# Optimization experiments

Hardware: AMD Instinct MI355X
Metric: run time of the kernel (lower is better)

Reference implementation:

```python
import jax, jax.numpy as jnp
import numpy as np

DIM = 2048       # model dim
HID = 1024       # expert hidden dim
E = 8            # num_experts
K = 2            # top_k
SHID = HID * 1   # shared expert hidden = hidden_dim * num_shared_experts
INIT = 0.02


def setup_inputs() -> dict:
    key = jax.random.key(0)
    ks = jax.random.split(key, 9)
    return {
        "x": jax.random.normal(ks[0], (2, 1024, DIM), jnp.float32),
        "expert_bias": jnp.zeros((E,), jnp.float32),
        "gate_w": jax.random.normal(ks[1], (E, DIM), jnp.float32) * INIT,
        "w1": jax.random.normal(ks[2], (E, HID, DIM), jnp.float32) * INIT,
        "w2": jax.random.normal(ks[3], (E, DIM, HID), jnp.float32) * INIT,
        "w3": jax.random.normal(ks[4], (E, HID, DIM), jnp.float32) * INIT,
        "sw1": jax.random.normal(ks[5], (SHID, DIM), jnp.float32) * INIT,
        "sw2": jax.random.normal(ks[6], (DIM, SHID), jnp.float32) * INIT,
        "sw3": jax.random.normal(ks[7], (SHID, DIM), jnp.float32) * INIT,
    }


def reference(x, expert_bias, gate_w, w1, w2, w3, sw1, sw2, sw3):
    B, S, D = x.shape
    xf = x.reshape(-1, D)                      # [N, D]
    N = xf.shape[0]

    # --- TokenChoiceTopKRouter (sigmoid score, bias-adjusted top-k selection) ---
    scores = jax.nn.sigmoid((xf @ gate_w.T).astype(jnp.float32))      # [N, E]
    _, sel = jax.lax.top_k(scores + expert_bias[None, :], K)          # [N, K] indices
    top_scores = jnp.take_along_axis(scores, sel, axis=1)             # [N, K] (route_norm=False, route_scale=1.0)

    # --- TokenReorderer: stable sort routed slots by expert id ---
    flat_exp = sel.reshape(-1)                                        # [N*K]
    order = jnp.argsort(flat_exp, stable=True)                        # expert-sorted slot order
    sorted_exp = flat_exp[order]                                      # [N*K]
    tok_idx = order // K                                              # source token per slot
    sc_sorted = top_scores.reshape(-1)[order]                         # [N*K]

    # score_before_experts=True: scale input by routing score before expert FFN
    rin = xf[tok_idx] * sc_sorted[:, None].astype(x.dtype)            # [N*K, D]

    # --- GroupedExperts: per-expert SwiGLU on the expert-sorted token block ---
    # (grouped GEMM expressed as a masked loop over the fixed expert set)
    out_sorted = jnp.zeros_like(rin)
    for e in range(E):
        m = (sorted_exp == e)[:, None].astype(rin.dtype)
        h = jax.nn.silu(rin @ w1[e].T) * (rin @ w3[e].T)              # [N*K, HID]
        out_sorted = out_sorted + m * (h @ w2[e].T)

    # combine: scatter-add expert outputs back to tokens
    routed = jnp.zeros((N, D), x.dtype).at[tok_idx].add(out_sorted)

    # shared expert (plain SwiGLU FeedForward)
    shared = (jax.nn.silu(xf @ sw1.T) * (xf @ sw3.T)) @ sw2.T

    return (routed + shared).reshape(B, S, D)
```

## Files before the change

### kernel.cpp

```cpp
#include <hip/hip_runtime.h>
#include <hip/hip_bf16.h>
#include <stdint.h>

#define DIMM 2048
#define HIDD 1024
#define NEXP 8
#define TOPK 2
#define NTOK 2048
#define CAP_E 1024
#define CAP_T (NEXP * CAP_E)

typedef __bf16 bf16_t;
typedef __bf16 bf16x4 __attribute__((ext_vector_type(4)));
typedef __bf16 bf16x8 __attribute__((ext_vector_type(8)));
typedef float f32x4 __attribute__((ext_vector_type(4)));

__device__ __forceinline__ void gl2lds16(const bf16_t* g, bf16_t* l) {
    __builtin_amdgcn_global_load_lds(
        (const __attribute__((address_space(1))) void*)g,
        (__attribute__((address_space(3))) void*)l, 16, 0, 0);
}

__global__ __launch_bounds__(256) void conv_f2b(const float* __restrict__ s,
                                                bf16_t* __restrict__ d, int n4) {
    int i = blockIdx.x * 256 + threadIdx.x;
    if (i >= n4) return;
    float4 v = ((const float4*)s)[i];
    bf16x4 o = {(bf16_t)v.x, (bf16_t)v.y, (bf16_t)v.z, (bf16_t)v.w};
    ((bf16x4*)d)[i] = o;
}

__global__ __launch_bounds__(256) void conv_w13(const float* __restrict__ w1,
                                                const float* __restrict__ w3,
                                                bf16_t* __restrict__ d, int n4) {
    int i = blockIdx.x * 256 + threadIdx.x;
    if (i >= n4) return;
    long flat = (long)i * 4;
    int e = (int)(flat >> 22);
    int rem = (int)(flat & ((1 << 22) - 1));
    int r = rem >> 11;
    int dd = rem & 2047;
    const float* src = (r < HIDD)
        ? (w1 + ((long)e << 21) + ((long)r << 11) + dd)
        : (w3 + ((long)e << 21) + ((long)(r - HIDD) << 11) + dd);
    float4 v = *(const float4*)src;
    bf16x4 o = {(bf16_t)v.x, (bf16_t)v.y, (bf16_t)v.z, (bf16_t)v.w};
    ((bf16x4*)d)[i] = o;
}

__global__ __launch_bounds__(256) void router_k(const float* __restrict__ x,
                                                const float* __restrict__ gw,
                                                const float* __restrict__ bias,
                                                int* __restrict__ sel,
                                                float* __restrict__ topsc) {
    int t = blockIdx.x;
    int tid = threadIdx.x;
    const float* xr = x + (long)t * DIMM;
    double acc[NEXP];
#pragma unroll
    for (int e = 0; e < NEXP; ++e) acc[e] = 0.0;
    for (int d = tid; d < DIMM; d += 256) {
        double xv = (double)xr[d];
#pragma unroll
        for (int e = 0; e < NEXP; ++e) acc[e] += xv * (double)gw[e * DIMM + d];
    }
#pragma unroll
    for (int off = 32; off >= 1; off >>= 1)
#pragma unroll
        for (int e = 0; e < NEXP; ++e) acc[e] += __shfl_down(acc[e], off, 64);
    __shared__ double red[4][NEXP];
    int lane = tid & 63, w = tid >> 6;
    if (lane == 0)
#pragma unroll
        for (int e = 0; e < NEXP; ++e) red[w][e] = acc[e];
    __syncthreads();
    if (tid == 0) {
        double sc[NEXP], v[NEXP];
#pragma unroll
        for (int e = 0; e < NEXP; ++e) {
            double s = red[0][e] + red[1][e] + red[2][e] + red[3][e];
            sc[e] = 1.0 / (1.0 + exp(-s));
            v[e] = sc[e] + (double)bias[e];
        }
        int b0 = 0;
        for (int e = 1; e < NEXP; ++e) if (v[e] > v[b0]) b0 = e;
        int b1 = -1;
        for (int e = 0; e < NEXP; ++e)
            if (e != b0 && (b1 < 0 || v[e] > v[b1])) b1 = e;
        sel[t * 2] = b0; sel[t * 2 + 1] = b1;
        topsc[t * 2] = (float)sc[b0]; topsc[t * 2 + 1] = (float)sc[b1];
    }
}

__global__ __launch_bounds__(256) void sort_k(const int* __restrict__ sel,
                                              const float* __restrict__ topsc,
                                              int* __restrict__ tok_s,
                                              float* __restrict__ sc_s,
                                              int* __restrict__ counts) {
    __shared__ int se[NTOK * TOPK];
    int tid = threadIdx.x;
    for (int i = tid; i < NTOK * TOPK; i += 256) se[i] = sel[i];
    __syncthreads();
    int wv = tid >> 6, lane = tid & 63;
    unsigned long long lower = (1ull << lane) - 1ull;
    for (int ei = 0; ei < 2; ++ei) {
        int e = wv * 2 + ei;
        int base = e * CAP_E;
        int off = 0;
        for (int c = 0; c < (NTOK * TOPK) / 64; ++c) {
            int slot = c * 64 + lane;
            bool m = (se[slot] == e);
            unsigned long long bal = __ballot(m);
            if (m) {
                int rank = off + __popcll(bal & lower);
                if (rank < CAP_E) {
                    tok_s[base + rank] = slot >> 1;
                    sc_s[base + rank] = topsc[slot];
                }
            }
            off += __popcll(bal);
        }
        int cnt = min(off, CAP_E);
        if (lane == 0) counts[e] = cnt;
        int padded = min((cnt + 127) & ~127, CAP_E);
        for (int r = cnt + lane; r < padded; r += 64) tok_s[base + r] = -1;
    }
}

__global__ __launch_bounds__(256) void build_rin(const float* __restrict__ x,
                                                 const int* __restrict__ tok_s,
                                                 const float* __restrict__ sc_s,
                                                 const int* __restrict__ counts,
                                                 bf16_t* __restrict__ rin) {
    int row = blockIdx.x;
    int e = row >> 10, r = row & (CAP_E - 1);
    int cnt = min(counts[e], CAP_E);
    int padded = min((cnt + 127) & ~127, CAP_E);
    if (r >= padded) return;
    int d0 = threadIdx.x * 8;
    bf16x8 o;
    if (r < cnt) {
        int tok = tok_s[row];
        float sc = sc_s[row];
        const float* src = x + (long)tok * DIMM + d0;
        float4 a = *(const float4*)src;
        float4 b = *(const float4*)(src + 4);
        o[0] = (bf16_t)(a.x * sc); o[1] = (bf16_t)(a.y * sc);
        o[2] = (bf16_t)(a.z * sc); o[3] = (bf16_t)(a.w * sc);
        o[4] = (bf16_t)(b.x * sc); o[5] = (bf16_t)(b.y * sc);
        o[6] = (bf16_t)(b.z * sc); o[7] = (bf16_t)(b.w * sc);
    } else {
#pragma unroll
        for (int i = 0; i < 8; ++i) o[i] = (bf16_t)0.0f;
    }
    *(bf16x8*)(rin + (long)row * DIMM + d0) = o;
}

template <int EPI>
__global__ __launch_bounds__(256, 2) void gemm_bt(
    const bf16_t* __restrict__ A0, const bf16_t* __restrict__ B0,
    void* __restrict__ C0, const int* __restrict__ counts, int Mfixed,
    int N, int K, long sA, long sB, long sC,
    const int* __restrict__ tok_s, float* __restrict__ outp) {
    int e = blockIdx.z;
    int M = Mfixed;
    if (counts) {
        int c = min(counts[e], Mfixed);
        M = min((c + 127) & ~127, Mfixed);
    }
    int m0 = blockIdx.y * 128;
    if (m0 >= M) return;
    int n0 = blockIdx.x * 128;
    const bf16_t* A = A0 + (long)e * sA;
    const bf16_t* B = B0 + (long)e * sB;

    __shared__ bf16_t lA[128 * 64];
    __shared__ bf16_t lB[128 * 64];

    int tid = threadIdx.x;
    int lane = tid & 63, wv = tid >> 6;
    int quad = lane >> 4, l16 = lane & 15;
    int wm = (wv & 1) * 64, wn = (wv >> 1) * 64;

    f32x4 acc[4][4];
#pragma unroll
    for (int i = 0; i < 4; ++i)
#pragma unroll
        for (int j = 0; j < 4; ++j) acc[i][j] = (f32x4){0.f, 0.f, 0.f, 0.f};

    int kTiles = K >> 6;
    for (int kt = 0; kt < kTiles; ++kt) {
        int kb = kt << 6;
#pragma unroll
        for (int i = 0; i < 4; ++i) {
            int q = i * 256 + tid;
            int row = q >> 3, cc = q & 7;
            int scc = cc ^ (row & 7);
            gl2lds16(A + (long)(m0 + row) * K + kb + scc * 8, &lA[q * 8]);
            gl2lds16(B + (long)(n0 + row) * K + kb + scc * 8, &lB[q * 8]);
        }
        __syncthreads();
#pragma unroll
        for (int ki = 0; ki < 2; ++ki) {
            bf16x8 af[4], bfr[4];
            int kc = ki * 4 + quad;
#pragma unroll
            for (int mi = 0; mi < 4; ++mi) {
                int row = wm + mi * 16 + l16;
                int chunk = row * 8 + (kc ^ (row & 7));
                af[mi] = *(const bf16x8*)&lA[chunk * 8];
            }
#pragma unroll
            for (int ni = 0; ni < 4; ++ni) {
                int row = wn + ni * 16 + l16;
                int chunk = row * 8 + (kc ^ (row & 7));
                bfr[ni] = *(const bf16x8*)&lB[chunk * 8];
            }
#pragma unroll
            for (int mi = 0; mi < 4; ++mi)
#pragma unroll
                for (int ni = 0; ni < 4; ++ni)
                    acc[mi][ni] = __builtin_amdgcn_mfma_f32_16x16x32_bf16(
                        af[mi], bfr[ni], acc[mi][ni], 0, 0, 0);
        }
        __syncthreads();
    }

    if (EPI == 0) {
        bf16_t* Cp = (bf16_t*)C0 + (long)e * sC;
#pragma unroll
        for (int mi = 0; mi < 4; ++mi)
#pragma unroll
            for (int r = 0; r < 4; ++r) {
                int row = m0 + wm + mi * 16 + quad * 4 + r;
#pragma unroll
                for (int ni = 0; ni < 4; ++ni) {
                    int col = n0 + wn + ni * 16 + l16;
                    Cp[(long)row * N + col] = (bf16_t)acc[mi][ni][r];
                }
            }
    } else if (EPI == 1) {
        float* Cp = (float*)C0;
#pragma unroll
        for (int mi = 0; mi < 4; ++mi)
#pragma unroll
            for (int r = 0; r < 4; ++r) {
                int row = m0 + wm + mi * 16 + quad * 4 + r;
#pragma unroll
                for (int ni = 0; ni < 4; ++ni) {
                    int col = n0 + wn + ni * 16 + l16;
                    Cp[(long)row * N + col] = acc[mi][ni][r];
                }
            }
    } else {
#pragma unroll
        for (int mi = 0; mi < 4; ++mi)
#pragma unroll
            for (int r = 0; r < 4; ++r) {
                int rloc = m0 + wm + mi * 16 + quad * 4 + r;
                int tok = tok_s[e * CAP_E + rloc];
                if (tok >= 0) {
                    float* op = outp + (long)tok * DIMM + n0 + wn + l16;
#pragma unroll
                    for (int ni = 0; ni < 4; ++ni)
                        atomicAdd(op + ni * 16, acc[mi][ni][r]);
                }
            }
    }
}

__global__ __launch_bounds__(256) void silu_comb(const bf16_t* __restrict__ ht,
                                                 bf16_t* __restrict__ h,
                                                 const int* __restrict__ counts) {
    int row = blockIdx.x;
    if (counts) {
        int e = row >> 10, r = row & (CAP_E - 1);
        int cnt = min(counts[e], CAP_E);
        int padded = min((cnt + 127) & ~127, CAP_E);
        if (r >= padded) return;
    }
    int j = threadIdx.x * 4;
    bf16x4 a4 = *(const bf16x4*)&ht[(long)row * 2048 + j];
    bf16x4 b4 = *(const bf16x4*)&ht[(long)row * 2048 + 1024 + j];
    bf16x4 o;
#pragma unroll
    for (int i = 0; i < 4; ++i) {
        float a = (float)a4[i], b = (float)b4[i];
        float s = a / (1.f + expf(-a));
        o[i] = (bf16_t)(s * b);
    }
    *(bf16x4*)&h[(long)row * 1024 + j] = o;
}

extern "C" void kernel_launch(void* const* d_in, const int* in_sizes, int n_in,
                              void* d_out, int out_size, void* d_ws, size_t ws_size,
                              hipStream_t stream) {
    const float* x    = (const float*)d_in[0];
    const float* bias = (const float*)d_in[1];
    const float* gw   = (const float*)d_in[2];
    const float* w1   = (const float*)d_in[3];
    const float* w2   = (const float*)d_in[4];
    const float* w3   = (const float*)d_in[5];
    const float* sw1  = (const float*)d_in[6];
    const float* sw2  = (const float*)d_in[7];
    const float* sw3  = (const float*)d_in[8];
    float* out = (float*)d_out;

    char* p = (char*)d_ws;
    auto alloc = [&](size_t bytes) {
        char* r = p;
        p += (bytes + 255) & ~(size_t)255;
        return r;
    };
    bf16_t* xb    = (bf16_t*)alloc((size_t)NTOK * DIMM * 2);
    bf16_t* w13b  = (bf16_t*)alloc((size_t)NEXP * 2048 * 2048 * 2);
    bf16_t* w2b   = (bf16_t*)alloc((size_t)NEXP * 2048 * 1024 * 2);
    bf16_t* sw13b = (bf16_t*)alloc((size_t)2048 * 2048 * 2);
    bf16_t* sw2b  = (bf16_t*)alloc((size_t)2048 * 1024 * 2);
    bf16_t* rin   = (bf16_t*)alloc((size_t)CAP_T * DIMM * 2);
    bf16_t* ht    = (bf16_t*)alloc((size_t)CAP_T * 2048 * 2);
    bf16_t* hB    = (bf16_t*)alloc((size_t)CAP_T * 1024 * 2);
    bf16_t* sht   = (bf16_t*)alloc((size_t)NTOK * 2048 * 2);
    bf16_t* shB   = (bf16_t*)alloc((size_t)NTOK * 1024 * 2);
    int*   sel    = (int*)alloc(NTOK * TOPK * 4);
    float* topsc  = (float*)alloc(NTOK * TOPK * 4);
    int*   tok_s  = (int*)alloc(CAP_T * 4);
    float* sc_s   = (float*)alloc(CAP_T * 4);
    int*   counts = (int*)alloc(256);

    int n4;
    n4 = NTOK * DIMM / 4;
    conv_f2b<<<n4 / 256, 256, 0, stream>>>(x, xb, n4);
    n4 = NEXP * 2048 * 2048 / 4;
    conv_w13<<<n4 / 256, 256, 0, stream>>>(w1, w3, w13b, n4);
    n4 = NEXP * 2048 * 1024 / 4;
    conv_f2b<<<n4 / 256, 256, 0, stream>>>(w2, w2b, n4);
    n4 = HIDD * 2048 / 4;
    conv_f2b<<<n4 / 256, 256, 0, stream>>>(sw1, sw13b, n4);
    conv_f2b<<<n4 / 256, 256, 0, stream>>>(sw3, sw13b + (size_t)HIDD * 2048, n4);
    n4 = 2048 * 1024 / 4;
    conv_f2b<<<n4 / 256, 256, 0, stream>>>(sw2, sw2b, n4);

    router_k<<<NTOK, 256, 0, stream>>>(x, gw, bias, sel, topsc);
    sort_k<<<1, 256, 0, stream>>>(sel, topsc, tok_s, sc_s, counts);
    build_rin<<<CAP_T, 256, 0, stream>>>(x, tok_s, sc_s, counts, rin);

    gemm_bt<0><<<dim3(16, CAP_E / 128, NEXP), 256, 0, stream>>>(
        rin, w13b, ht, counts, CAP_E, 2048, 2048,
        (long)CAP_E * 2048, (long)2048 * 2048, (long)CAP_E * 2048, nullptr, nullptr);
    gemm_bt<0><<<dim3(16, 16, 1), 256, 0, stream>>>(
        xb, sw13b, sht, nullptr, 2048, 2048, 2048, 0, 0, 0, nullptr, nullptr);

    silu_comb<<<CAP_T, 256, 0, stream>>>(ht, hB, counts);
    silu_comb<<<NTOK, 256, 0, stream>>>(sht, shB, nullptr);

    gemm_bt<1><<<dim3(16, 16, 1), 256, 0, stream>>>(
        shB, sw2b, out, nullptr, 2048, 2048, 1024, 0, 0, 0, nullptr, nullptr);
    gemm_bt<2><<<dim3(16, CAP_E / 128, NEXP), 256, 0, stream>>>(
        hB, w2b, nullptr, counts, CAP_E, 2048, 1024,
        (long)CAP_E * 1024, (long)2048 * 1024, 0, tok_s, out);
}
```

Baseline: 516.7 us.

## Fuse fp32-to-bf16 weight conversion into GEMM loads and batch shared expert as group

Drops the separate weight-conversion kernels and instead loads fp32 weights directly inside the GEMM main loop, converting them to bf16 in registers before writing to LDS. The shared expert is folded in as a ninth group of the grouped GEMM, so both phases run in one launch each. The output is zeroed up front and all results are atomically accumulated. This removes the extra passes that read fp32 weights and wrote bf16 copies to memory. The cost is that B tiles are now loaded synchronously through registers rather than by direct global-to-LDS loads, and twice the bytes of weights are read per tile, with repeated reads across M-tiles.

Result: faster. 479.4 us (-7.2%).

```diff
diff --git a/kernel.cpp b/kernel.cpp
--- a/kernel.cpp
+++ b/kernel.cpp
@@ -8,7 +8,8 @@
 #define TOPK 2
 #define NTOK 2048
 #define CAP_E 1024
-#define CAP_T (NEXP * CAP_E)
+#define SH_BASE (NEXP * CAP_E)
+#define NROW (SH_BASE + NTOK)
 
 typedef __bf16 bf16_t;
 typedef __bf16 bf16x4 __attribute__((ext_vector_type(4)));
@@ -21,31 +22,9 @@
         (__attribute__((address_space(3))) void*)l, 16, 0, 0);
 }
 
-__global__ __launch_bounds__(256) void conv_f2b(const float* __restrict__ s,
-                                                bf16_t* __restrict__ d, int n4) {
+__global__ __launch_bounds__(256) void zero_f(float* __restrict__ p, int n4) {
     int i = blockIdx.x * 256 + threadIdx.x;
-    if (i >= n4) return;
-    float4 v = ((const float4*)s)[i];
-    bf16x4 o = {(bf16_t)v.x, (bf16_t)v.y, (bf16_t)v.z, (bf16_t)v.w};
-    ((bf16x4*)d)[i] = o;
-}
-
-__global__ __launch_bounds__(256) void conv_w13(const float* __restrict__ w1,
-                                                const float* __restrict__ w3,
-                                                bf16_t* __restrict__ d, int n4) {
-    int i = blockIdx.x * 256 + threadIdx.x;
-    if (i >= n4) return;
-    long flat = (long)i * 4;
-    int e = (int)(flat >> 22);
-    int rem = (int)(flat & ((1 << 22) - 1));
-    int r = rem >> 11;
-    int dd = rem & 2047;
-    const float* src = (r < HIDD)
-        ? (w1 + ((long)e << 21) + ((long)r << 11) + dd)
-        : (w3 + ((long)e << 21) + ((long)(r - HIDD) << 11) + dd);
-    float4 v = *(const float4*)src;
-    bf16x4 o = {(bf16_t)v.x, (bf16_t)v.y, (bf16_t)v.z, (bf16_t)v.w};
-    ((bf16x4*)d)[i] = o;
+    if (i < n4) ((float4*)p)[i] = (float4){0.f, 0.f, 0.f, 0.f};
 }
 
 __global__ __launch_bounds__(256) void router_k(const float* __restrict__ x,
@@ -133,15 +112,20 @@
                                                  const int* __restrict__ counts,
                                                  bf16_t* __restrict__ rin) {
     int row = blockIdx.x;
-    int e = row >> 10, r = row & (CAP_E - 1);
-    int cnt = min(counts[e], CAP_E);
-    int padded = min((cnt + 127) & ~127, CAP_E);
-    if (r >= padded) return;
+    int tok; float sc = 1.0f;
+    if (row >= SH_BASE) {
+        tok = row - SH_BASE;
+    } else {
+        int e = row >> 10, r = row & (CAP_E - 1);
+        int cnt = min(counts[e], CAP_E);
+        int padded = min((cnt + 127) & ~127, CAP_E);
+        if (r >= padded) return;
+        if (r < cnt) { tok = tok_s[row]; sc = sc_s[row]; }
+        else tok = -1;
+    }
     int d0 = threadIdx.x * 8;
     bf16x8 o;
-    if (r < cnt) {
-        int tok = tok_s[row];
-        float sc = sc_s[row];
+    if (tok >= 0) {
         const float* src = x + (long)tok * DIMM + d0;
         float4 a = *(const float4*)src;
         float4 b = *(const float4*)(src + 4);
@@ -156,23 +140,25 @@
     *(bf16x8*)(rin + (long)row * DIMM + d0) = o;
 }
 
-template <int EPI>
-__global__ __launch_bounds__(256, 2) void gemm_bt(
-    const bf16_t* __restrict__ A0, const bf16_t* __restrict__ B0,
-    void* __restrict__ C0, const int* __restrict__ counts, int Mfixed,
-    int N, int K, long sA, long sB, long sC,
-    const int* __restrict__ tok_s, float* __restrict__ outp) {
-    int e = blockIdx.z;
-    int M = Mfixed;
-    if (counts) {
-        int c = min(counts[e], Mfixed);
-        M = min((c + 127) & ~127, Mfixed);
+template <int PHASE>
+__global__ __launch_bounds__(256, 2) void gemm_moe(
+    const bf16_t* __restrict__ A0,
+    const float* __restrict__ W1, const float* __restrict__ W3,
+    const float* __restrict__ SW1, const float* __restrict__ SW3,
+    bf16_t* __restrict__ Cout, float* __restrict__ outp,
+    const int* __restrict__ counts, const int* __restrict__ tok_s) {
+    constexpr int K = (PHASE == 1) ? 2048 : 1024;
+    int g = blockIdx.z;
+    int base = (g < 8) ? g * CAP_E : SH_BASE;
+    int M = NTOK;
+    if (g < 8) {
+        int c = min(counts[g], CAP_E);
+        M = min((c + 127) & ~127, CAP_E);
     }
     int m0 = blockIdx.y * 128;
     if (m0 >= M) return;
     int n0 = blockIdx.x * 128;
-    const bf16_t* A = A0 + (long)e * sA;
-    const bf16_t* B = B0 + (long)e * sB;
+    const bf16_t* A = A0 + (long)base * K;
 
     __shared__ bf16_t lA[128 * 64];
     __shared__ bf16_t lB[128 * 64];
@@ -181,6 +167,28 @@
     int lane = tid & 63, wv = tid >> 6;
     int quad = lane >> 4, l16 = lane & 15;
     int wm = (wv & 1) * 64, wn = (wv >> 1) * 64;
+    int cc = tid & 7;
+    int rbase = tid >> 3;
+
+    const float* brow[4];
+    int slot[4];
+#pragma unroll
+    for (int i = 0; i < 4; ++i) {
+        int row = i * 32 + rbase;
+        int n = n0 + row;
+        const float* p;
+        if (PHASE == 1) {
+            if (g < 8) p = (n < HIDD) ? W1 + ((long)g << 21) + (long)n * DIMM
+                                      : W3 + ((long)g << 21) + (long)(n - HIDD) * DIMM;
+            else       p = (n < HIDD) ? SW1 + (long)n * DIMM
+                                      : SW3 + (long)(n - HIDD) * DIMM;
+        } else {
+            p = (g < 8) ? W1 + ((long)g << 21) + (long)n * HIDD
+                        : SW1 + (long)n * HIDD;
+        }
+        brow[i] = p + cc * 8;
+        slot[i] = row * 8 + (cc ^ (row & 7));
+    }
 
     f32x4 acc[4][4];
 #pragma unroll
@@ -188,16 +196,26 @@
 #pragma unroll
         for (int j = 0; j < 4; ++j) acc[i][j] = (f32x4){0.f, 0.f, 0.f, 0.f};
 
-    int kTiles = K >> 6;
-    for (int kt = 0; kt < kTiles; ++kt) {
-        int kb = kt << 6;
+    for (int kt = 0; kt < K / 64; ++kt) {
+        int kb = kt * 64;
 #pragma unroll
         for (int i = 0; i < 4; ++i) {
-            int q = i * 256 + tid;
-            int row = q >> 3, cc = q & 7;
+            int row = i * 32 + rbase;
             int scc = cc ^ (row & 7);
-            gl2lds16(A + (long)(m0 + row) * K + kb + scc * 8, &lA[q * 8]);
-            gl2lds16(B + (long)(n0 + row) * K + kb + scc * 8, &lB[q * 8]);
+            gl2lds16(A + (long)(m0 + row) * K + kb + scc * 8, &lA[(i * 256 + tid) * 8]);
+        }
+        float4 u[4], v[4];
+#pragma unroll
+        for (int i = 0; i < 4; ++i) {
+            const float* p = brow[i] + kb;
+            u[i] = *(const float4*)p;
+            v[i] = *(const float4*)(p + 4);
+        }
+#pragma unroll
+        for (int i = 0; i < 4; ++i) {
+            bf16x8 o = {(bf16_t)u[i].x, (bf16_t)u[i].y, (bf16_t)u[i].z, (bf16_t)u[i].w,
+                        (bf16_t)v[i].x, (bf16_t)v[i].y, (bf16_t)v[i].z, (bf16_t)v[i].w};
+            *(bf16x8*)&lB[slot[i] * 8] = o;
         }
         __syncthreads();
 #pragma unroll
@@ -226,30 +244,16 @@
         __syncthreads();
     }
 
-    if (EPI == 0) {
-        bf16_t* Cp = (bf16_t*)C0 + (long)e * sC;
+    if (PHASE == 1) {
 #pragma unroll
         for (int mi = 0; mi < 4; ++mi)
 #pragma unroll
             for (int r = 0; r < 4; ++r) {
-                int row = m0 + wm + mi * 16 + quad * 4 + r;
+                int row = base + m0 + wm + mi * 16 + quad * 4 + r;
 #pragma unroll
                 for (int ni = 0; ni < 4; ++ni) {
                     int col = n0 + wn + ni * 16 + l16;
-                    Cp[(long)row * N + col] = (bf16_t)acc[mi][ni][r];
-                }
-            }
-    } else if (EPI == 1) {
-        float* Cp = (float*)C0;
-#pragma unroll
-        for (int mi = 0; mi < 4; ++mi)
-#pragma unroll
-            for (int r = 0; r < 4; ++r) {
-                int row = m0 + wm + mi * 16 + quad * 4 + r;
-#pragma unroll
-                for (int ni = 0; ni < 4; ++ni) {
-                    int col = n0 + wn + ni * 16 + l16;
-                    Cp[(long)row * N + col] = acc[mi][ni][r];
+                    Cout[(long)row * DIMM + col] = (bf16_t)acc[mi][ni][r];
                 }
             }
     } else {
@@ -258,7 +262,7 @@
 #pragma unroll
             for (int r = 0; r < 4; ++r) {
                 int rloc = m0 + wm + mi * 16 + quad * 4 + r;
-                int tok = tok_s[e * CAP_E + rloc];
+                int tok = (g < 8) ? tok_s[g * CAP_E + rloc] : rloc;
                 if (tok >= 0) {
                     float* op = outp + (long)tok * DIMM + n0 + wn + l16;
 #pragma unroll
@@ -273,15 +277,15 @@
                                                  bf16_t* __restrict__ h,
                                                  const int* __restrict__ counts) {
     int row = blockIdx.x;
-    if (counts) {
+    if (row < SH_BASE) {
         int e = row >> 10, r = row & (CAP_E - 1);
         int cnt = min(counts[e], CAP_E);
         int padded = min((cnt + 127) & ~127, CAP_E);
         if (r >= padded) return;
     }
     int j = threadIdx.x * 4;
-    bf16x4 a4 = *(const bf16x4*)&ht[(long)row * 2048 + j];
-    bf16x4 b4 = *(const bf16x4*)&ht[(long)row * 2048 + 1024 + j];
+    bf16x4 a4 = *(const bf16x4*)&ht[(long)row * DIMM + j];
+    bf16x4 b4 = *(const bf16x4*)&ht[(long)row * DIMM + HIDD + j];
     bf16x4 o;
 #pragma unroll
     for (int i = 0; i < 4; ++i) {
@@ -289,7 +293,7 @@
         float s = a / (1.f + expf(-a));
         o[i] = (bf16_t)(s * b);
     }
-    *(bf16x4*)&h[(long)row * 1024 + j] = o;
+    *(bf16x4*)&h[(long)row * HIDD + j] = o;
 }
 
 extern "C" void kernel_launch(void* const* d_in, const int* in_sizes, int n_in,
@@ -312,51 +316,25 @@
         p += (bytes + 255) & ~(size_t)255;
         return r;
     };
-    bf16_t* xb    = (bf16_t*)alloc((size_t)NTOK * DIMM * 2);
-    bf16_t* w13b  = (bf16_t*)alloc((size_t)NEXP * 2048 * 2048 * 2);
-    bf16_t* w2b   = (bf16_t*)alloc((size_t)NEXP * 2048 * 1024 * 2);
-    bf16_t* sw13b = (bf16_t*)alloc((size_t)2048 * 2048 * 2);
-    bf16_t* sw2b  = (bf16_t*)alloc((size_t)2048 * 1024 * 2);
-    bf16_t* rin   = (bf16_t*)alloc((size_t)CAP_T * DIMM * 2);
-    bf16_t* ht    = (bf16_t*)alloc((size_t)CAP_T * 2048 * 2);
-    bf16_t* hB    = (bf16_t*)alloc((size_t)CAP_T * 1024 * 2);
-    bf16_t* sht   = (bf16_t*)alloc((size_t)NTOK * 2048 * 2);
-    bf16_t* shB   = (bf16_t*)alloc((size_t)NTOK * 1024 * 2);
+    bf16_t* rin   = (bf16_t*)alloc((size_t)NROW * DIMM * 2);
+    bf16_t* ht    = (bf16_t*)alloc((size_t)NROW * DIMM * 2);
+    bf16_t* hB    = (bf16_t*)alloc((size_t)NROW * HIDD * 2);
     int*   sel    = (int*)alloc(NTOK * TOPK * 4);
     float* topsc  = (float*)alloc(NTOK * TOPK * 4);
-    int*   tok_s  = (int*)alloc(CAP_T * 4);
-    float* sc_s   = (float*)alloc(CAP_T * 4);
+    int*   tok_s  = (int*)alloc(SH_BASE * 4);
+    float* sc_s   = (float*)alloc(SH_BASE * 4);
     int*   counts = (int*)alloc(256);
 
-    int n4;
-    n4 = NTOK * DIMM / 4;
-    conv_f2b<<<n4 / 256, 256, 0, stream>>>(x, xb, n4);
-    n4 = NEXP * 2048 * 2048 / 4;
-    conv_w13<<<n4 / 256, 256, 0, stream>>>(w1, w3, w13b, n4);
-    n4 = NEXP * 2048 * 1024 / 4;
-    conv_f2b<<<n4 / 256, 256, 0, stream>>>(w2, w2b, n4);
-    n4 = HIDD * 2048 / 4;
-    conv_f2b<<<n4 / 256, 256, 0, stream>>>(sw1, sw13b, n4);
-    conv_f2b<<<n4 / 256, 256, 0, stream>>>(sw3, sw13b + (size_t)HIDD * 2048, n4);
-    n4 = 2048 * 1024 / 4;
-    conv_f2b<<<n4 / 256, 256, 0, stream>>>(sw2, sw2b, n4);
-
+    zero_f<<<(NTOK * DIMM / 4) / 256, 256, 0, stream>>>(out, NTOK * DIMM / 4);
     router_k<<<NTOK, 256, 0, stream>>>(x, gw, bias, sel, topsc);
     sort_k<<<1, 256, 0, stream>>>(sel, topsc, tok_s, sc_s, counts);
-    build_rin<<<CAP_T, 256, 0, stream>>>(x, tok_s, sc_s, counts, rin);
-
-    gemm_bt<0><<<dim3(16, CAP_E / 128, NEXP), 256, 0, stream>>>(
-        rin, w13b, ht, counts, CAP_E, 2048, 2048,
-        (long)CAP_E * 2048, (long)2048 * 2048, (long)CAP_E * 2048, nullptr, nullptr);
-    gemm_bt<0><<<dim3(16, 16, 1), 256, 0, stream>>>(
-        xb, sw13b, sht, nullptr, 2048, 2048, 2048, 0, 0, 0, nullptr, nullptr);
-
-    silu_comb<<<CAP_T, 256, 0, stream>>>(ht, hB, counts);
-    silu_comb<<<NTOK, 256, 0, stream>>>(sht, shB, nullptr);
-
-    gemm_bt<1><<<dim3(16, 16, 1), 256, 0, stream>>>(
-        shB, sw2b, out, nullptr, 2048, 2048, 1024, 0, 0, 0, nullptr, nullptr);
-    gemm_bt<2><<<dim3(16, CAP_E / 128, NEXP), 256, 0, stream>>>(
-        hB, w2b, nullptr, counts, CAP_E, 2048, 1024,
-        (long)CAP_E * 1024, (long)2048 * 1024, 0, tok_s, out);
-}
+    build_rin<<<NROW, 256, 0, stream>>>(x, tok_s, sc_s, counts, rin);
+
+    gemm_moe<1><<<dim3(16, 16, 9), 256, 0, stream>>>(
+        rin, w1, w3, sw1, sw3, ht, nullptr, counts, nullptr);
+
+    silu_comb<<<NROW, 256, 0, stream>>>(ht, hB, counts);
+
+    gemm_moe<2><<<dim3(16, 16, 9), 256, 0, stream>>>(
+        hB, w2, nullptr, sw2, nullptr, nullptr, out, counts, tok_s);
+}
```
